# Kernel optimization log

Hardware: AMD Instinct MI355X
Metric: run time of the kernel (lower is better)

The kernel has to match this reference:

```python
import jax, jax.numpy as jnp
import numpy as np

SCALE = 32.0
MARGIN = 0.25


def setup_inputs() -> dict:
    key = jax.random.key(0)
    k1, k2 = jax.random.split(key)
    feats = jax.random.normal(k1, (8192, 128), dtype=jnp.float32)
    labels = jax.random.randint(k2, (8192,), 0, 14, dtype=jnp.int64)
    return {"feats": feats, "labels": labels}


def reference(feats, labels):
    # cosine similarity: L2-normalize rows then GEMM  -> sim [B, B]
    f = feats / jnp.linalg.norm(feats, axis=1, keepdims=True)
    sim = f @ f.T

    B = feats.shape[0]
    same = labels[:, None] == labels[None, :]
    eye = jnp.eye(B, dtype=bool)
    pos_mask = same & ~eye          # same label, excluding self
    neg_mask = ~same                # different label

    s, m = SCALE, MARGIN
    alpha_p = jax.nn.relu(1.0 + m - sim)
    alpha_n = jax.nn.relu(sim + m)
    # exponents; masked-out entries set to -inf so exp -> 0 (matches masked sum)
    expo_p = jnp.where(pos_mask, -s * alpha_p * (sim - (1.0 - m)), -jnp.inf)
    expo_n = jnp.where(neg_mask, s * alpha_n * (sim - m), -jnp.inf)

    loss_p = jnp.sum(jnp.exp(expo_p), axis=1)   # [B]
    loss_n = jnp.sum(jnp.exp(expo_n), axis=1)   # [B]
    loss = jnp.mean(jnp.log1p(loss_p * loss_n))
    return loss
```

## Files before the change

### kernel.cpp

```cpp
#include <hip/hip_runtime.h>
#include <math.h>


#define DIM 128
typedef short bf16x8 __attribute__((ext_vector_type(8)));
typedef float f32x4 __attribute__((ext_vector_type(4)));

#if __has_builtin(__builtin_amdgcn_exp2f)
#define EXP2F __builtin_amdgcn_exp2f
#else
#define EXP2F exp2f
#endif

__device__ __forceinline__ unsigned short f2bf(float f) {
    unsigned int b = __float_as_uint(f);
    unsigned int r = (b + 0x7FFFu + ((b >> 16) & 1u)) >> 16;
    return (unsigned short)r;
}
__device__ __forceinline__ unsigned int packPN(float p, float n) {
    return (unsigned int)f2bf(p) | ((unsigned int)f2bf(n) << 16);
}

__global__ void prep_kernel(const float* __restrict__ feats,
                            unsigned int* __restrict__ featsN, int B) {
    int wave = (blockIdx.x * blockDim.x + threadIdx.x) >> 6;
    int lane = threadIdx.x & 63;
    if (wave >= B) return;
    const float2* rp = (const float2*)(feats + (size_t)wave * DIM);
    float2 v = rp[lane];
    float s = v.x * v.x + v.y * v.y;
#pragma unroll
    for (int off = 32; off; off >>= 1) s += __shfl_xor(s, off);
    float inv = rsqrtf(s);
    featsN[(size_t)wave * 64 + lane] =
        (unsigned int)f2bf(v.x * inv) | ((unsigned int)f2bf(v.y * inv) << 16);
}

__global__ __launch_bounds__(256, 2) void circle_main_kernel(
    const unsigned short* __restrict__ featsN, const int* __restrict__ labels,
    unsigned int* __restrict__ partial, int B) {
    __shared__ unsigned char smem[65536] __attribute__((aligned(16)));
    unsigned char* Al = smem;
    unsigned char* Bl = smem + 32768;
    float2* tbuf = (float2*)smem;

    int bid = blockIdx.x;
    int RT = (int)((129.0 - sqrt(16641.0 - 8.0 * (double)bid)) * 0.5);
    RT = RT < 0 ? 0 : (RT > 63 ? 63 : RT);
    while (64 * RT - (RT * (RT - 1)) / 2 > bid) --RT;
    while (64 * (RT + 1) - ((RT + 1) * RT) / 2 <= bid) ++RT;
    const int CT = RT + (bid - (64 * RT - (RT * (RT - 1)) / 2));
    const bool diag = (RT == CT);

    const int tid = threadIdx.x;
    const int lane = tid & 63;
    const int wv = tid >> 6;
    const int wr = wv >> 1, wc = wv & 1;
    const int lg = lane >> 4;
    const int l15 = lane & 15;

    {
        const int r0 = tid >> 4, c = tid & 15;
#pragma unroll
        for (int it = 0; it < 8; ++it) {
            int row = it * 16 + r0;
            int swz = ((c ^ (row & 15)) << 4);
            int4 va = *(const int4*)(featsN + (size_t)(RT * 128 + row) * DIM + c * 8);
            *(int4*)(Al + row * 256 + swz) = va;
            int4 vb = *(const int4*)(featsN + (size_t)(CT * 128 + row) * DIM + c * 8);
            *(int4*)(Bl + row * 256 + swz) = vb;
        }
    }
    __syncthreads();

    f32x4 acc[4][4];
#pragma unroll
    for (int m = 0; m < 4; ++m)
#pragma unroll
        for (int n = 0; n < 4; ++n) acc[m][n] = (f32x4){0.f, 0.f, 0.f, 0.f};
#pragma unroll
    for (int kk = 0; kk < 4; ++kk) {
        bf16x8 af[4], bfr[4];
#pragma unroll
        for (int m = 0; m < 4; ++m) {
            int row = wr * 64 + m * 16 + l15;
            af[m] = __builtin_bit_cast(bf16x8,
                *(const int4*)(Al + row * 256 + (((kk * 4 + lg) ^ (row & 15)) << 4)));
        }
#pragma unroll
        for (int n = 0; n < 4; ++n) {
            int row = wc * 64 + n * 16 + l15;
            bfr[n] = __builtin_bit_cast(bf16x8,
                *(const int4*)(Bl + row * 256 + (((kk * 4 + lg) ^ (row & 15)) << 4)));
        }
#pragma unroll
        for (int m = 0; m < 4; ++m)
#pragma unroll
            for (int n = 0; n < 4; ++n)
                acc[m][n] = __builtin_amdgcn_mfma_f32_16x16x32_bf16(
                    af[m], bfr[n], acc[m][n], 0, 0, 0);
    }

    const int rowbase = RT * 128 + wr * 64;
    const int colbase = CT * 128 + wc * 64;
    const float S2 = 46.166241308446828f;
    const float C2 = -23.083120654223414f;

    int lc[4], lr[4][4];
#pragma unroll
    for (int n = 0; n < 4; ++n) lc[n] = labels[colbase + n * 16 + l15];
#pragma unroll
    for (int m = 0; m < 4; ++m)
#pragma unroll
        for (int r = 0; r < 4; ++r) lr[m][r] = labels[rowbase + m * 16 + lg * 4 + r];

    float rN[4][4], rP[4][4];
    float cN[4] = {0.f, 0.f, 0.f, 0.f}, cP[4] = {0.f, 0.f, 0.f, 0.f};

    if (diag) {
#pragma unroll
        for (int m = 0; m < 4; ++m) {
#pragma unroll
            for (int r = 0; r < 4; ++r) {
                const int grow = rowbase + m * 16 + lg * 4 + r;
                const int lrow = lr[m][r];
                float psum = 0.f, nsum = 0.f;
#pragma unroll
                for (int n = 0; n < 4; ++n) {
                    float sim = acc[m][n][r];
                    bool same = (lrow == lc[n]);
                    float u = same ? (1.25f - sim) : (sim + 0.25f);
                    float e2 = fmaxf(u, 0.f) * fmaf(S2, u, C2);
                    float v = EXP2F(e2);
                    bool self = (grow == colbase + n * 16 + l15);
                    float pv = (same && !self) ? v : 0.f;
                    float nv = same ? 0.f : v;
                    psum += pv; nsum += nv;
                }
                rP[m][r] = psum; rN[m][r] = nsum;
            }
        }
    } else {
#pragma unroll
        for (int m = 0; m < 4; ++m) {
#pragma unroll
            for (int r = 0; r < 4; ++r) {
                const int lrow = lr[m][r];
                float psum = 0.f, nsum = 0.f;
#pragma unroll
                for (int n = 0; n < 4; ++n) {
                    float sim = acc[m][n][r];
                    bool same = (lrow == lc[n]);
                    float u = same ? (1.25f - sim) : (sim + 0.25f);
                    float e2 = fmaxf(u, 0.f) * fmaf(S2, u, C2);
                    float v = EXP2F(e2);
                    float pv = same ? v : 0.f;
                    float nv = v - pv;
                    psum += pv; nsum += nv;
                    cP[n] += pv; cN[n] += nv;
                }
                rP[m][r] = psum; rN[m][r] = nsum;
            }
        }
    }

    if (!diag) {
#pragma unroll
        for (int n = 0; n < 4; ++n) {
            float p = cP[n], n_ = cN[n];
            p += __shfl_xor(p, 16); p += __shfl_xor(p, 32);
            n_ += __shfl_xor(n_, 16); n_ += __shfl_xor(n_, 32);
            if (lg == 0) {
                int gcol = colbase + n * 16 + l15;
                partial[(size_t)(RT * 2 + wr) * B + gcol] = packPN(p, n_);
            }
        }
    }

    __syncthreads();
    {
        float2* T = tbuf + wv * 64 * 17;
#pragma unroll
        for (int m = 0; m < 4; ++m)
#pragma unroll
            for (int r = 0; r < 4; ++r)
                T[(m * 16 + lg * 4 + r) * 17 + l15] =
                    make_float2(rP[m][r], rN[m][r]);
    }
    __syncthreads();
    {
        const float2* T = tbuf + wv * 64 * 17 + lane * 17;
        float p = 0.f, n_ = 0.f;
#pragma unroll
        for (int c = 0; c < 16; ++c) {
            float2 t = T[c];
            p += t.x; n_ += t.y;
        }
        int grow = RT * 128 + wr * 64 + lane;
        partial[(size_t)(CT * 2 + wc) * B + grow] = packPN(p, n_);
    }
}

__global__ void rowloss_kernel(const unsigned int* __restrict__ partial,
                               double* __restrict__ blocksum, int B) {
    __shared__ double sdata[256];
    int tid = threadIdx.x;
    int row = blockIdx.x * 256 + tid;
    float p = 0.f, n = 0.f;
#pragma unroll
    for (int c = 0; c < 128; ++c) {
        unsigned int v = partial[(size_t)c * B + row];
        p += __uint_as_float(v << 16);
        n += __uint_as_float(v & 0xFFFF0000u);
    }
    sdata[tid] = log1p((double)p * (double)n);
    __syncthreads();
    for (int s = 128; s; s >>= 1) {
        if (tid < s) sdata[tid] += sdata[tid + s];
        __syncthreads();
    }
    if (tid == 0) blocksum[blockIdx.x] = sdata[0];
}

__global__ void final_kernel(const double* __restrict__ blocksum,
                             float* __restrict__ out, int nblk, int B) {
    __shared__ double sdata[64];
    int tid = threadIdx.x;
    sdata[tid] = (tid < nblk) ? blocksum[tid] : 0.0;
    __syncthreads();
    for (int s = 32; s; s >>= 1) {
        if (tid < s) sdata[tid] += sdata[tid + s];
        __syncthreads();
    }
    if (tid == 0) out[0] = (float)(sdata[0] / (double)B);
}

extern "C" void kernel_launch(void* const* d_in, const int* in_sizes, int n_in,
                              void* d_out, int out_size, void* d_ws, size_t ws_size,
                              hipStream_t stream) {
    const float* feats = (const float*)d_in[0];
    const int* labels = (const int*)d_in[1];
    float* out = (float*)d_out;
    int B = in_sizes[1];

    unsigned int* featsN = (unsigned int*)d_ws;
    size_t off1 = ((size_t)B * DIM * 2 + 255) & ~(size_t)255;
    unsigned int* partial = (unsigned int*)((char*)d_ws + off1);
    size_t off2 = off1 + (((size_t)B * 128 * sizeof(unsigned int) + 255) & ~(size_t)255);
    double* blocksum = (double*)((char*)d_ws + off2);

    prep_kernel<<<B / 4, 256, 0, stream>>>(feats, featsN, B);

    int ntiles = B / 128;
    int nblocks = ntiles * (ntiles + 1) / 2;
    circle_main_kernel<<<nblocks, 256, 0, stream>>>((const unsigned short*)featsN,
                                                    labels, partial, B);

    int nblk = B / 256;
    rowloss_kernel<<<nblk, 256, 0, stream>>>(partial, blocksum, B);
    final_kernel<<<1, 64, 0, stream>>>(blocksum, out, nblk, B);
}
```

Before: 44.00 us.

## Pack row partials, vectorize P/N accumulation, and parallelize rowloss over columns

The main kernel now accumulates positive and negative sums as two-wide float vectors, which may map to packed FP32 adds. The per-wave row transpose buffer stores bf16-packed pairs instead of float2, halving its LDS traffic. The rowloss kernel now has four wave-groups each summing a quarter of the 128 partial columns for 64 rows, then combines them through LDS and a wave shuffle. This launches four times more rowloss blocks, and final_kernel is widened to 128 threads to match. Rounding the per-row partials to bf16 before the cross-lane sum adds precision loss.

```diff
diff --git a/kernel.cpp b/kernel.cpp
--- a/kernel.cpp
+++ b/kernel.cpp
@@ -5,6 +5,7 @@
 #define DIM 128
 typedef short bf16x8 __attribute__((ext_vector_type(8)));
 typedef float f32x4 __attribute__((ext_vector_type(4)));
+typedef float f32x2 __attribute__((ext_vector_type(2)));
 
 #if __has_builtin(__builtin_amdgcn_exp2f)
 #define EXP2F __builtin_amdgcn_exp2f
@@ -42,7 +43,7 @@
     __shared__ unsigned char smem[65536] __attribute__((aligned(16)));
     unsigned char* Al = smem;
     unsigned char* Bl = smem + 32768;
-    float2* tbuf = (float2*)smem;
+    unsigned int* tbuf = (unsigned int*)smem;
 
     int bid = blockIdx.x;
     int RT = (int)((129.0 - sqrt(16641.0 - 8.0 * (double)bid)) * 0.5);
@@ -114,8 +115,9 @@
 #pragma unroll
         for (int r = 0; r < 4; ++r) lr[m][r] = labels[rowbase + m * 16 + lg * 4 + r];
 
-    float rN[4][4], rP[4][4];
-    float cN[4] = {0.f, 0.f, 0.f, 0.f}, cP[4] = {0.f, 0.f, 0.f, 0.f};
+    f32x2 rPN[4][4];
+    f32x2 cPN[4] = {(f32x2){0.f, 0.f}, (f32x2){0.f, 0.f},
+                    (f32x2){0.f, 0.f}, (f32x2){0.f, 0.f}};
 
     if (diag) {
 #pragma unroll
@@ -124,7 +126,7 @@
             for (int r = 0; r < 4; ++r) {
                 const int grow = rowbase + m * 16 + lg * 4 + r;
                 const int lrow = lr[m][r];
-                float psum = 0.f, nsum = 0.f;
+                f32x2 s_ = (f32x2){0.f, 0.f};
 #pragma unroll
                 for (int n = 0; n < 4; ++n) {
                     float sim = acc[m][n][r];
@@ -133,11 +135,11 @@
                     float e2 = fmaxf(u, 0.f) * fmaf(S2, u, C2);
                     float v = EXP2F(e2);
                     bool self = (grow == colbase + n * 16 + l15);
-                    float pv = (same && !self) ? v : 0.f;
-                    float nv = same ? 0.f : v;
-                    psum += pv; nsum += nv;
+                    v = self ? 0.f : v;
+                    float pv = same ? v : 0.f;
+                    s_ += (f32x2){pv, v - pv};
                 }
-                rP[m][r] = psum; rN[m][r] = nsum;
+                rPN[m][r] = s_;
             }
         }
     } else {
@@ -146,7 +148,7 @@
 #pragma unroll
             for (int r = 0; r < 4; ++r) {
                 const int lrow = lr[m][r];
-                float psum = 0.f, nsum = 0.f;
+                f32x2 s_ = (f32x2){0.f, 0.f};
 #pragma unroll
                 for (int n = 0; n < 4; ++n) {
                     float sim = acc[m][n][r];
@@ -155,11 +157,11 @@
                     float e2 = fmaxf(u, 0.f) * fmaf(S2, u, C2);
                     float v = EXP2F(e2);
                     float pv = same ? v : 0.f;
-                    float nv = v - pv;
-                    psum += pv; nsum += nv;
-                    cP[n] += pv; cN[n] += nv;
+                    f32x2 w = (f32x2){pv, v - pv};
+                    s_ += w;
+                    cPN[n] += w;
                 }
-                rP[m][r] = psum; rN[m][r] = nsum;
+                rPN[m][r] = s_;
             }
         }
     }
@@ -167,7 +169,7 @@
     if (!diag) {
 #pragma unroll
         for (int n = 0; n < 4; ++n) {
-            float p = cP[n], n_ = cN[n];
+            float p = cPN[n].x, n_ = cPN[n].y;
             p += __shfl_xor(p, 16); p += __shfl_xor(p, 32);
             n_ += __shfl_xor(n_, 16); n_ += __shfl_xor(n_, 32);
             if (lg == 0) {
@@ -179,22 +181,22 @@
 
     __syncthreads();
     {
-        float2* T = tbuf + wv * 64 * 17;
+        unsigned int* T = tbuf + wv * 64 * 17;
 #pragma unroll
         for (int m = 0; m < 4; ++m)
 #pragma unroll
             for (int r = 0; r < 4; ++r)
-                T[(m * 16 + lg * 4 + r) * 17 + l15] =
-                    make_float2(rP[m][r], rN[m][r]);
+                T[(m * 16 + lg * 4 + r) * 17 + l15] = packPN(rPN[m][r].x, rPN[m][r].y);
     }
     __syncthreads();
     {
-        const float2* T = tbuf + wv * 64 * 17 + lane * 17;
+        const unsigned int* T = tbuf + wv * 64 * 17 + lane * 17;
         float p = 0.f, n_ = 0.f;
 #pragma unroll
         for (int c = 0; c < 16; ++c) {
-            float2 t = T[c];
-            p += t.x; n_ += t.y;
+            unsigned int v = T[c];
+            p += __uint_as_float(v << 16);
+            n_ += __uint_as_float(v & 0xFFFF0000u);
         }
         int grow = RT * 128 + wr * 64 + lane;
         partial[(size_t)(CT * 2 + wc) * B + grow] = packPN(p, n_);
@@ -203,32 +205,38 @@
 
 __global__ void rowloss_kernel(const unsigned int* __restrict__ partial,
                                double* __restrict__ blocksum, int B) {
-    __shared__ double sdata[256];
+    __shared__ float2 sdata[64][4];
     int tid = threadIdx.x;
-    int row = blockIdx.x * 256 + tid;
+    int r6 = tid & 63, q = tid >> 6;
+    int row = blockIdx.x * 64 + r6;
     float p = 0.f, n = 0.f;
 #pragma unroll
-    for (int c = 0; c < 128; ++c) {
+    for (int c = q * 32; c < q * 32 + 32; ++c) {
         unsigned int v = partial[(size_t)c * B + row];
         p += __uint_as_float(v << 16);
         n += __uint_as_float(v & 0xFFFF0000u);
     }
-    sdata[tid] = log1p((double)p * (double)n);
-    __syncthreads();
-    for (int s = 128; s; s >>= 1) {
-        if (tid < s) sdata[tid] += sdata[tid + s];
-        __syncthreads();
-    }
-    if (tid == 0) blocksum[blockIdx.x] = sdata[0];
+    sdata[r6][q] = make_float2(p, n);
+    __syncthreads();
+    if (q == 0) {
+        float2 a0 = sdata[r6][0], a1 = sdata[r6][1];
+        float2 a2 = sdata[r6][2], a3 = sdata[r6][3];
+        double pf = (double)(a0.x + a1.x + a2.x + a3.x);
+        double nf = (double)(a0.y + a1.y + a2.y + a3.y);
+        double l = log1p(pf * nf);
+#pragma unroll
+        for (int off = 32; off; off >>= 1) l += __shfl_xor(l, off);
+        if (r6 == 0) blocksum[blockIdx.x] = l;
+    }
 }
 
 __global__ void final_kernel(const double* __restrict__ blocksum,
                              float* __restrict__ out, int nblk, int B) {
-    __shared__ double sdata[64];
+    __shared__ double sdata[128];
     int tid = threadIdx.x;
     sdata[tid] = (tid < nblk) ? blocksum[tid] : 0.0;
     __syncthreads();
-    for (int s = 32; s; s >>= 1) {
+    for (int s = 64; s; s >>= 1) {
         if (tid < s) sdata[tid] += sdata[tid + s];
         __syncthreads();
     }
@@ -256,7 +264,7 @@
     circle_main_kernel<<<nblocks, 256, 0, stream>>>((const unsigned short*)featsN,
                                                     labels, partial, B);
 
-    int nblk = B / 256;
+    int nblk = B / 64;
     rowloss_kernel<<<nblk, 256, 0, stream>>>(partial, blocksum, B);
-    final_kernel<<<1, 64, 0, stream>>>(blocksum, out, nblk, B);
-}
+    final_kernel<<<1, 128, 0, stream>>>(blocksum, out, nblk, B);
+}
```

After: 42.38 us, median of 2. 1.04x faster.
